# Kernel optimization log

Measured on AMD Instinct MI355X. Metric: run time of the kernel, lower is better.

The kernel has to match this reference:

```python
import jax, jax.numpy as jnp
import numpy as np

D_K = 64
N_HEADS = 12
LN_EPS = 1e-5


def layer_norm(x, eps=LN_EPS):
    # nn.LayerNorm(768) is created fresh each forward -> weight=1, bias=0
    mu = jnp.mean(x, axis=-1, keepdims=True)
    var = jnp.mean(jnp.square(x - mu), axis=-1, keepdims=True)
    return (x - mu) * jax.lax.rsqrt(var + eps)


def setup_inputs() -> dict:
    key = jax.random.key(0)
    ks = jax.random.split(key, 7)
    B, S, D = 2, 2048, 768
    scale = 1.0 / np.sqrt(D)
    return {
        "input_Q": jax.random.normal(ks[0], (B, S, D), jnp.float32),
        "input_K": jax.random.normal(ks[1], (B, S, D), jnp.float32),
        "input_V": jax.random.normal(ks[2], (B, S, D), jnp.float32),
        "Wq": jax.random.normal(ks[3], (D, D), jnp.float32) * scale,
        "Wk": jax.random.normal(ks[4], (D, D), jnp.float32) * scale,
        "Wv": jax.random.normal(ks[5], (D, D), jnp.float32) * scale,
        "Wo": jax.random.normal(ks[6], (D, D), jnp.float32) * scale,
    }


def reference(input_Q, input_K, input_V, Wq, Wk, Wv, Wo):
    B, Sq, D = input_Q.shape
    Sk = input_K.shape[1]
    H, dk = N_HEADS, D_K
    residual = input_Q
    # projections: [B,S,D] @ [D, H*dk] -> [B,H,S,dk]
    Q = (input_Q @ Wq).reshape(B, Sq, H, dk).transpose(0, 2, 1, 3)
    K = (input_K @ Wk).reshape(B, Sk, H, dk).transpose(0, 2, 1, 3)
    V = (input_V @ Wv).reshape(B, Sk, H, dk).transpose(0, 2, 1, 3)
    # attention scores [B,H,Sq,Sk]
    att = jnp.einsum("bhqd,bhkd->bhqk", Q, K) / np.sqrt(dk).astype(np.float32)
    att = jax.nn.softmax(att, axis=-1)
    ctx = jnp.einsum("bhqk,bhkd->bhqd", att, V)  # [B,H,Sq,dk]
    ctx = ctx.transpose(0, 2, 1, 3).reshape(B, Sq, H * dk)
    out = ctx @ Wo
    return layer_norm(out + residual)
```

## Files before the change

### kernel.cpp

```cpp
#include <hip/hip_runtime.h>
#include <hip/hip_bf16.h>
#include <stdint.h>

#define S_LEN 2048
#define D_MODEL 768
#define NH 12
#define DK 64
#define BATCH 2
#define M_TOT (BATCH * S_LEN)

typedef __attribute__((ext_vector_type(8))) short short8;
typedef __attribute__((ext_vector_type(4))) float f32x4;
typedef __attribute__((ext_vector_type(16))) float f32x16;

__device__ inline short f2bf(float f) {
  union { float f; uint32_t u; } v; v.f = f;
  uint32_t r = v.u + 0x7fffu + ((v.u >> 16) & 1u);
  return (short)(r >> 16);
}

__device__ inline f32x4 mfma16(short8 a, short8 b, f32x4 c) {
  return __builtin_amdgcn_mfma_f32_16x16x32_bf16(a, b, c, 0, 0, 0);
}
__device__ inline f32x16 mfma32(short8 a, short8 b, f32x16 c) {
  return __builtin_amdgcn_mfma_f32_32x32x16_bf16(a, b, c, 0, 0, 0);
}

__device__ inline void gl16(const void* g, void* l) {
  __builtin_amdgcn_global_load_lds(
      (const __attribute__((address_space(1))) unsigned*)g,
      (__attribute__((address_space(3))) unsigned*)l, 16, 0, 0);
}

__device__ inline unsigned cvtpk(float lo, float hi) {
  unsigned r;
  asm("v_cvt_pk_bf16_f32 %0, %1, %2" : "=v"(r) : "v"(lo), "v"(hi));
  return r;
}
__device__ inline void plswap(unsigned& a, unsigned& b) {
  asm("v_permlane32_swap_b32 %0, %1" : "+v"(a), "+v"(b));
}
__device__ inline float lo16(uint32_t u) {
  union { uint32_t u; float f; } x; x.u = u << 16; return x.f;
}
__device__ inline float hi16(uint32_t u) {
  union { uint32_t u; float f; } x; x.u = u & 0xffff0000u; return x.f;
}

__global__ __launch_bounds__(256) void transpose_w_kernel(
    const float* __restrict__ Wq, const float* __restrict__ Wk,
    const float* __restrict__ Wv, const float* __restrict__ Wo,
    short* __restrict__ WT) {
  int z = blockIdx.z;
  const float* W = z == 0 ? Wq : (z == 1 ? Wk : (z == 2 ? Wv : Wo));
  short* O = WT + (size_t)z * D_MODEL * D_MODEL;
  __shared__ float t[32][33];
  int x = threadIdx.x, y = threadIdx.y;
  int nb = blockIdx.x * 32, kb = blockIdx.y * 32;
#pragma unroll
  for (int j = 0; j < 4; ++j)
    t[y + 8 * j][x] = W[(kb + y + 8 * j) * D_MODEL + nb + x];
  __syncthreads();
#pragma unroll
  for (int j = 0; j < 4; ++j)
    O[(nb + y + 8 * j) * D_MODEL + kb + x] = f2bf(t[x][y + 8 * j]);
}

__global__ __launch_bounds__(256) void cast_x_kernel(
    const float* __restrict__ Xq, const float* __restrict__ Xk,
    const float* __restrict__ Xv, short* __restrict__ Xb) {
  int z = blockIdx.y;
  const float* X = z == 0 ? Xq : (z == 1 ? Xk : Xv);
  short* O = Xb + (size_t)z * M_TOT * D_MODEL;
  size_t i = ((size_t)blockIdx.x * 256 + threadIdx.x) * 8;
  float4 f0 = *(const float4*)(X + i);
  float4 f1 = *(const float4*)(X + i + 4);
  short8 v;
  v[0] = f2bf(f0.x); v[1] = f2bf(f0.y); v[2] = f2bf(f0.z); v[3] = f2bf(f0.w);
  v[4] = f2bf(f1.x); v[5] = f2bf(f1.y); v[6] = f2bf(f1.z); v[7] = f2bf(f1.w);
  *(short8*)(O + i) = v;
}

__global__ __launch_bounds__(256) void proj_kernel(
    const short* __restrict__ Xb, const short* __restrict__ WTall,
    short* __restrict__ Qo, short* __restrict__ Ko, short* __restrict__ Vo) {
  int bid = blockIdx.x;
  int wk = (bid & 7) * 72 + (bid >> 3);
  int which = wk / 192;
  int rem = wk % 192;
  int mt = rem / 6, nt = rem % 6;
  int mbase = mt * 128, nbase = nt * 128;
  const short* X = Xb + (size_t)which * M_TOT * D_MODEL;
  const short* WT = WTall + (size_t)which * D_MODEL * D_MODEL;

  __shared__ short As[128][32];
  __shared__ short Bs[128][32];
  int tid = threadIdx.x;
  int wv = tid >> 6, lane = tid & 63, r = lane & 15, g = lane >> 4;
  int wm = (wv & 1) * 64, wn = (wv >> 1) * 64;
  int srow = (lane >> 2), scol = (lane & 3) * 8;

  f32x4 acc[4][4] = {};
  for (int kk = 0; kk < D_MODEL; kk += 32) {
#pragma unroll
    for (int j = 0; j < 2; ++j) {
      int row = wv * 32 + j * 16;
      gl16(X + (size_t)(mbase + row + srow) * D_MODEL + kk + scol, &As[row][0]);
      gl16(WT + (size_t)(nbase + row + srow) * D_MODEL + kk + scol, &Bs[row][0]);
    }
    __syncthreads();
    short8 a[4], b[4];
#pragma unroll
    for (int i = 0; i < 4; ++i) {
      a[i] = *(short8*)&As[wm + i * 16 + r][g * 8];
      b[i] = *(short8*)&Bs[wn + i * 16 + r][g * 8];
    }
#pragma unroll
    for (int i = 0; i < 4; ++i)
#pragma unroll
      for (int j = 0; j < 4; ++j)
        acc[i][j] = mfma16(a[i], b[j], acc[i][j]);
    __syncthreads();
  }
#pragma unroll
  for (int i = 0; i < 4; ++i)
#pragma unroll
    for (int j = 0; j < 4; ++j)
#pragma unroll
      for (int reg = 0; reg < 4; ++reg) {
        int m = mbase + wm + i * 16 + g * 4 + reg;
        int n = nbase + wn + j * 16 + r;
        int b_ = m >> 11, s = m & 2047, h = n >> 6, d = n & 63;
        if (which == 0) {
          short v = f2bf(acc[i][j][reg] * 0.18033688f);
          Qo[(((size_t)b_ * NH + h) * S_LEN + s) * DK + d] = v;
        } else if (which == 1) {
          short v = f2bf(acc[i][j][reg]);
          Ko[(((size_t)b_ * NH + h) * S_LEN + s) * DK + (d ^ ((s & 7) << 3))] = v;
        } else {
          short v = f2bf(acc[i][j][reg]);
          Vo[(((size_t)b_ * NH + h) * DK + d) * S_LEN + (s ^ ((d & 7) << 3))] = v;
        }
      }
}

__global__ __launch_bounds__(128) void attn_kernel(
    const short* __restrict__ Qg, const short* __restrict__ Kg,
    const short* __restrict__ Vt, short* __restrict__ oP,
    float* __restrict__ mlP) {
  __shared__ char K_lds[2][8192];
  __shared__ char V_lds[2][8192];
  int bh = blockIdx.y;
  int split = blockIdx.z;
  int tid = threadIdx.x;
  int w = tid >> 6, lane = tid & 63;
  int c32 = lane & 31, hi = lane >> 5;
  int qbase = blockIdx.x * 64 + w * 32;
  int kc0 = split * (S_LEN / 2);
  const short* qp = Qg + (size_t)bh * S_LEN * DK;
  const char* kp = (const char*)(Kg + (size_t)bh * S_LEN * DK);
  const char* vp = (const char*)(Vt + (size_t)bh * DK * S_LEN);

  short8 qf[4];
#pragma unroll
  for (int kk = 0; kk < 4; ++kk)
    qf[kk] = *(const short8*)(qp + (size_t)(qbase + c32) * DK + kk * 16 + hi * 8);

#define STAGE(buf, kc)                                                          \
  {                                                                             \
    _Pragma("unroll") for (int j = 0; j < 4; ++j) {                             \
      int p = w * 4 + j;                                                        \
      gl16(kp + (size_t)(kc)*128 + p * 1024 + lane * 16, &K_lds[buf][p * 1024]);\
    }                                                                           \
    _Pragma("unroll") for (int j = 0; j < 4; ++j) {                             \
      int p = w * 4 + j;                                                        \
      int row = p * 8 + (lane >> 3);                                            \
      gl16(vp + (size_t)row * 4096 + (kc)*2 + (lane & 7) * 16,                  \
           &V_lds[buf][p * 1024]);                                              \
    }                                                                           \
  }

  STAGE(0, kc0);

  f32x16 o0 = {}, o1 = {};
  float m_run = -30000.f, l_run = 0.f;
  int cur = 0;
  const int NT = (S_LEN / 2) / 64;

  for (int t = 0; t < NT; ++t) {
    if (t < NT - 1) {
      STAGE(cur ^ 1, kc0 + (t + 1) * 64);
      asm volatile("s_waitcnt vmcnt(8)" ::: "memory");
    } else {
      asm volatile("s_waitcnt vmcnt(0)" ::: "memory");
    }
    __builtin_amdgcn_s_barrier();

    const char* kb = K_lds[cur];
    const char* vb = V_lds[cur];

    f32x16 st0 = {}, st1 = {};
#pragma unroll
    for (int kk = 0; kk < 4; ++kk) {
      int cb = kk * 32 + hi * 16;
      short8 k0 = *(const short8*)(kb + c32 * 128 + (cb ^ ((c32 & 7) << 4)));
      short8 k1 = *(const short8*)(kb + (32 + c32) * 128 + (cb ^ ((c32 & 7) << 4)));
      st0 = mfma32(k0, qf[kk], st0);
      st1 = mfma32(k1, qf[kk], st1);
    }

    float cm = -30000.f;
#pragma unroll
    for (int i = 0; i < 16; ++i) cm = fmaxf(cm, fmaxf(st0[i], st1[i]));
    cm = fmaxf(cm, __shfl_xor(cm, 32));
    if (!__all(cm <= m_run + 8.0f)) {
      float m_new = fmaxf(m_run, cm);
      float al = __builtin_amdgcn_exp2f(m_run - m_new);
      l_run *= al;
      m_run = m_new;
#pragma unroll
      for (int r = 0; r < 16; ++r) {
        int ql = (r & 3) + 8 * (r >> 2) + 4 * hi;
        float ar = __shfl(al, ql);
        o0[r] *= ar;
        o1[r] *= ar;
      }
    }
    float csum = 0.f;
#pragma unroll
    for (int i = 0; i < 16; ++i) {
      st0[i] = __builtin_amdgcn_exp2f(st0[i] - m_run);
      st1[i] = __builtin_amdgcn_exp2f(st1[i] - m_run);
      csum += st0[i] + st1[i];
    }
    csum += __shfl_xor(csum, 32);
    l_run += csum;

#pragma unroll
    for (int ks = 0; ks < 4; ++ks) {
      f32x16 P = (ks < 2) ? st0 : st1;
      int s8 = (ks & 1) * 8;
      unsigned A = cvtpk(P[s8 + 0], P[s8 + 1]);
      unsigned Bx = cvtpk(P[s8 + 4], P[s8 + 5]);
      unsigned C = cvtpk(P[s8 + 2], P[s8 + 3]);
      unsigned Dx = cvtpk(P[s8 + 6], P[s8 + 7]);
      plswap(A, Bx);
      plswap(C, Dx);
      union { unsigned u[4]; short8 s; } pu;
      pu.u[0] = A; pu.u[1] = C; pu.u[2] = Bx; pu.u[3] = Dx;
      int cb = ks * 32 + hi * 16;
      short8 v0 = *(const short8*)(vb + c32 * 128 + (cb ^ ((c32 & 7) << 4)));
      short8 v1 = *(const short8*)(vb + (32 + c32) * 128 + (cb ^ ((c32 & 7) << 4)));
      o0 = mfma32(pu.s, v0, o0);
      o1 = mfma32(pu.s, v1, o1);
    }

    __builtin_amdgcn_s_barrier();
    cur ^= 1;
  }

  size_t pbase = ((size_t)split * 24 + bh) * S_LEN;
#pragma unroll
  for (int r = 0; r < 16; ++r) {
    int ql = (r & 3) + 8 * (r >> 2) + 4 * hi;
    float linv = 1.0f / __shfl(l_run, ql);
    short* op = oP + (pbase + qbase + ql) * DK;
    op[c32] = f2bf(o0[r] * linv);
    op[32 + c32] = f2bf(o1[r] * linv);
  }
  if (hi == 0) {
    float* mlp = mlP + (pbase + qbase + c32) * 2;
    mlp[0] = m_run;
    mlp[1] = l_run;
  }
#undef STAGE
}

__global__ __launch_bounds__(256) void merge_kernel(
    const short* __restrict__ oP, const float* __restrict__ mlP,
    short* __restrict__ Cx) {
  int t = blockIdx.x * 256 + threadIdx.x;
  int q = t >> 5, dp = (t & 31) * 2;
  const int NQ = 24 * S_LEN;
  float2 ml0 = *(const float2*)(mlP + (size_t)q * 2);
  float2 ml1 = *(const float2*)(mlP + ((size_t)NQ + q) * 2);
  float m = fmaxf(ml0.x, ml1.x);
  float a0 = ml0.y * __builtin_amdgcn_exp2f(ml0.x - m);
  float a1 = ml1.y * __builtin_amdgcn_exp2f(ml1.x - m);
  float inv = 1.0f / (a0 + a1);
  float w0 = a0 * inv, w1 = a1 * inv;
  uint32_t a = *(const uint32_t*)(oP + (size_t)q * DK + dp);
  uint32_t b2 = *(const uint32_t*)(oP + ((size_t)NQ + q) * DK + dp);
  float v0 = lo16(a) * w0 + lo16(b2) * w1;
  float v1 = hi16(a) * w0 + hi16(b2) * w1;
  int bh = q >> 11, sr = q & 2047, b = bh / NH, h = bh % NH;
  uint32_t outw = (uint32_t)(uint16_t)f2bf(v0) | ((uint32_t)(uint16_t)f2bf(v1) << 16);
  *(uint32_t*)(Cx + ((size_t)(b * S_LEN + sr)) * D_MODEL + h * DK + dp) = outw;
}

__global__ __launch_bounds__(256) void gemm_out_kernel(
    const short* __restrict__ ctx, const short* __restrict__ WoT,
    const float* __restrict__ resid, float* __restrict__ Y) {
  int bid = blockIdx.x;
  int wk = (bid & 7) * 24 + (bid >> 3);
  int mt = wk / 6, nt = wk % 6;
  int mbase = mt * 128, nbase = nt * 128;

  __shared__ short As[128][32];
  __shared__ short Bs[128][32];
  int tid = threadIdx.x;
  int wv = tid >> 6, lane = tid & 63, r = lane & 15, g = lane >> 4;
  int wm = (wv & 1) * 64, wn = (wv >> 1) * 64;
  int srow = (lane >> 2), scol = (lane & 3) * 8;

  f32x4 acc[4][4] = {};
  for (int kk = 0; kk < D_MODEL; kk += 32) {
#pragma unroll
    for (int j = 0; j < 2; ++j) {
      int row = wv * 32 + j * 16;
      gl16(ctx + (size_t)(mbase + row + srow) * D_MODEL + kk + scol, &As[row][0]);
      gl16(WoT + (size_t)(nbase + row + srow) * D_MODEL + kk + scol, &Bs[row][0]);
    }
    __syncthreads();
    short8 a[4], b[4];
#pragma unroll
    for (int i = 0; i < 4; ++i) {
      a[i] = *(short8*)&As[wm + i * 16 + r][g * 8];
      b[i] = *(short8*)&Bs[wn + i * 16 + r][g * 8];
    }
#pragma unroll
    for (int i = 0; i < 4; ++i)
#pragma unroll
      for (int j = 0; j < 4; ++j)
        acc[i][j] = mfma16(a[i], b[j], acc[i][j]);
    __syncthreads();
  }
#pragma unroll
  for (int i = 0; i < 4; ++i)
#pragma unroll
    for (int j = 0; j < 4; ++j)
#pragma unroll
      for (int reg = 0; reg < 4; ++reg) {
        int m = mbase + wm + i * 16 + g * 4 + reg;
        int n = nbase + wn + j * 16 + r;
        Y[(size_t)m * D_MODEL + n] = acc[i][j][reg] + resid[(size_t)m * D_MODEL + n];
      }
}

__global__ __launch_bounds__(256) void ln_kernel(const float* __restrict__ Y,
                                                 float* __restrict__ out) {
  int row = blockIdx.x * 4 + (threadIdx.x >> 6);
  int l = threadIdx.x & 63;
  const float* yp = Y + (size_t)row * D_MODEL;
  float v[12];
  float s = 0.f, q = 0.f;
#pragma unroll
  for (int c = 0; c < 12; ++c) {
    v[c] = yp[c * 64 + l];
    s += v[c];
    q += v[c] * v[c];
  }
#pragma unroll
  for (int d = 1; d < 64; d <<= 1) {
    s += __shfl_xor(s, d);
    q += __shfl_xor(q, d);
  }
  float mu = s * (1.0f / 768.0f);
  float var = q * (1.0f / 768.0f) - mu * mu;
  float rstd = rsqrtf(var + 1e-5f);
  float* op = out + (size_t)row * D_MODEL;
#pragma unroll
  for (int c = 0; c < 12; ++c)
    op[c * 64 + l] = (v[c] - mu) * rstd;
}

extern "C" void kernel_launch(void* const* d_in, const int* in_sizes, int n_in,
                              void* d_out, int out_size, void* d_ws, size_t ws_size,
                              hipStream_t stream) {
  const float* xq = (const float*)d_in[0];
  const float* xk = (const float*)d_in[1];
  const float* xv = (const float*)d_in[2];
  const float* Wq = (const float*)d_in[3];
  const float* Wk = (const float*)d_in[4];
  const float* Wv = (const float*)d_in[5];
  const float* Wo = (const float*)d_in[6];
  float* out = (float*)d_out;

  char* ws = (char*)d_ws;
  const size_t WSZ = (size_t)D_MODEL * D_MODEL;
  const size_t QSZ = (size_t)M_TOT * D_MODEL;
  short* WT = (short*)ws;
  short* Xb = WT + 4 * WSZ;
  short* Qb = Xb + 3 * QSZ;
  short* Kb = Qb + QSZ;
  short* Vb = Kb + QSZ;
  short* Cx = Vb + QSZ;
  short* oP = Xb;
  float* mlP = (float*)(Xb + (size_t)2 * 24 * S_LEN * DK);
  float* Yf = (float*)Xb;

  transpose_w_kernel<<<dim3(24, 24, 4), dim3(32, 8), 0, stream>>>(Wq, Wk, Wv, Wo, WT);
  cast_x_kernel<<<dim3(1536, 3), 256, 0, stream>>>(xq, xk, xv, Xb);
  proj_kernel<<<576, 256, 0, stream>>>(Xb, WT, Qb, Kb, Vb);
  attn_kernel<<<dim3(32, 24, 2), 128, 0, stream>>>(Qb, Kb, Vb, oP, mlP);
  merge_kernel<<<6144, 256, 0, stream>>>(oP, mlP, Cx);
  gemm_out_kernel<<<192, 256, 0, stream>>>(Cx, WT + 3 * WSZ, xq, Yf);
  ln_kernel<<<1024, 256, 0, stream>>>(Yf, out);
}
```

Baseline: 233.3 us.

## Load K/V tiles directly from global memory instead of LDS double buffering

The attention kernel drops its LDS double-buffered K/V staging and has each wave read swizzled K and transposed-V fragments straight from global memory (relying on L1/L2), which also removes the per-tile barriers. Blocks grow from 2 to 4 waves covering 128 queries, halving the grid along the query axis. This removes LDS traffic and synchronisation but exposes global-load latency on every tile with no explicit prefetch, and each wave now fetches K/V redundantly through cache.

```diff
diff --git a/kernel.cpp b/kernel.cpp
--- a/kernel.cpp
+++ b/kernel.cpp
@@ -144,18 +144,16 @@
       }
 }
 
-__global__ __launch_bounds__(128) void attn_kernel(
+__global__ __launch_bounds__(256) void attn_kernel(
     const short* __restrict__ Qg, const short* __restrict__ Kg,
     const short* __restrict__ Vt, short* __restrict__ oP,
     float* __restrict__ mlP) {
-  __shared__ char K_lds[2][8192];
-  __shared__ char V_lds[2][8192];
   int bh = blockIdx.y;
   int split = blockIdx.z;
   int tid = threadIdx.x;
   int w = tid >> 6, lane = tid & 63;
   int c32 = lane & 31, hi = lane >> 5;
-  int qbase = blockIdx.x * 64 + w * 32;
+  int qbase = blockIdx.x * 128 + w * 32;
   int kc0 = split * (S_LEN / 2);
   const short* qp = Qg + (size_t)bh * S_LEN * DK;
   const char* kp = (const char*)(Kg + (size_t)bh * S_LEN * DK);
@@ -166,47 +164,32 @@
   for (int kk = 0; kk < 4; ++kk)
     qf[kk] = *(const short8*)(qp + (size_t)(qbase + c32) * DK + kk * 16 + hi * 8);
 
-#define STAGE(buf, kc)                                                          \
-  {                                                                             \
-    _Pragma("unroll") for (int j = 0; j < 4; ++j) {                             \
-      int p = w * 4 + j;                                                        \
-      gl16(kp + (size_t)(kc)*128 + p * 1024 + lane * 16, &K_lds[buf][p * 1024]);\
-    }                                                                           \
-    _Pragma("unroll") for (int j = 0; j < 4; ++j) {                             \
-      int p = w * 4 + j;                                                        \
-      int row = p * 8 + (lane >> 3);                                            \
-      gl16(vp + (size_t)row * 4096 + (kc)*2 + (lane & 7) * 16,                  \
-           &V_lds[buf][p * 1024]);                                              \
-    }                                                                           \
-  }
-
-  STAGE(0, kc0);
-
   f32x16 o0 = {}, o1 = {};
   float m_run = -30000.f, l_run = 0.f;
-  int cur = 0;
   const int NT = (S_LEN / 2) / 64;
+  int sw = (c32 & 7) << 4;
 
   for (int t = 0; t < NT; ++t) {
-    if (t < NT - 1) {
-      STAGE(cur ^ 1, kc0 + (t + 1) * 64);
-      asm volatile("s_waitcnt vmcnt(8)" ::: "memory");
-    } else {
-      asm volatile("s_waitcnt vmcnt(0)" ::: "memory");
-    }
-    __builtin_amdgcn_s_barrier();
-
-    const char* kb = K_lds[cur];
-    const char* vb = V_lds[cur];
+    int kc = kc0 + t * 64;
+    const char* kt = kp + (size_t)kc * 128;
+    const char* vt = vp + (size_t)kc * 2;
 
     f32x16 st0 = {}, st1 = {};
 #pragma unroll
     for (int kk = 0; kk < 4; ++kk) {
       int cb = kk * 32 + hi * 16;
-      short8 k0 = *(const short8*)(kb + c32 * 128 + (cb ^ ((c32 & 7) << 4)));
-      short8 k1 = *(const short8*)(kb + (32 + c32) * 128 + (cb ^ ((c32 & 7) << 4)));
+      short8 k0 = *(const short8*)(kt + (size_t)c32 * 128 + (cb ^ sw));
+      short8 k1 = *(const short8*)(kt + (size_t)(32 + c32) * 128 + (cb ^ sw));
       st0 = mfma32(k0, qf[kk], st0);
       st1 = mfma32(k1, qf[kk], st1);
+    }
+
+    short8 vl0[4], vl1[4];
+#pragma unroll
+    for (int ks = 0; ks < 4; ++ks) {
+      int cb = ks * 32 + hi * 16;
+      vl0[ks] = *(const short8*)(vt + (size_t)c32 * 4096 + (cb ^ sw));
+      vl1[ks] = *(const short8*)(vt + (size_t)(32 + c32) * 4096 + (cb ^ sw));
     }
 
     float cm = -30000.f;
@@ -248,15 +231,9 @@
       plswap(C, Dx);
       union { unsigned u[4]; short8 s; } pu;
       pu.u[0] = A; pu.u[1] = C; pu.u[2] = Bx; pu.u[3] = Dx;
-      int cb = ks * 32 + hi * 16;
-      short8 v0 = *(const short8*)(vb + c32 * 128 + (cb ^ ((c32 & 7) << 4)));
-      short8 v1 = *(const short8*)(vb + (32 + c32) * 128 + (cb ^ ((c32 & 7) << 4)));
-      o0 = mfma32(pu.s, v0, o0);
-      o1 = mfma32(pu.s, v1, o1);
-    }
-
-    __builtin_amdgcn_s_barrier();
-    cur ^= 1;
+      o0 = mfma32(pu.s, vl0[ks], o0);
+      o1 = mfma32(pu.s, vl1[ks], o1);
+    }
   }
 
   size_t pbase = ((size_t)split * 24 + bh) * S_LEN;
@@ -273,7 +250,6 @@
     mlp[0] = m_run;
     mlp[1] = l_run;
   }
-#undef STAGE
 }
 
 __global__ __launch_bounds__(256) void merge_kernel(
@@ -402,7 +378,7 @@
   transpose_w_kernel<<<dim3(24, 24, 4), dim3(32, 8), 0, stream>>>(Wq, Wk, Wv, Wo, WT);
   cast_x_kernel<<<dim3(1536, 3), 256, 0, stream>>>(xq, xk, xv, Xb);
   proj_kernel<<<576, 256, 0, stream>>>(Xb, WT, Qb, Kb, Vb);
-  attn_kernel<<<dim3(32, 24, 2), 128, 0, stream>>>(Qb, Kb, Vb, oP, mlP);
+  attn_kernel<<<dim3(16, 24, 2), 256, 0, stream>>>(Qb, Kb, Vb, oP, mlP);
   merge_kernel<<<6144, 256, 0, stream>>>(oP, mlP, Cx);
   gemm_out_kernel<<<192, 256, 0, stream>>>(Cx, WT + 3 * WSZ, xq, Yf);
   ln_kernel<<<1024, 256, 0, stream>>>(Yf, out);
```

New measurement: 223.7 us. -4.1%, faster.
